# Kernel tuning notes

Measured on AMD Instinct MI355X. Metric: run time of the kernel, lower is better.

## Reference

```python
import jax, jax.numpy as jnp
import numpy as np
import math

B, T, C, H = 4, 2048, 1024, 16
D = C // H  # head dim = 64
W_STD = 0.02


def setup_inputs() -> dict:
    key = jax.random.key(0)
    kx, kw, kb = jax.random.split(key, 3)
    x = jax.random.normal(kx, (B, T, C), dtype=jnp.float32)
    # Linear params stored as [in, 3*in] for x @ W; scaled like typical init
    w_qkv = jax.random.normal(kw, (C, 3 * C), dtype=jnp.float32) * W_STD
    b_qkv = jax.random.normal(kb, (3 * C,), dtype=jnp.float32) * W_STD
    return {"x": x, "w_qkv": w_qkv, "b_qkv": b_qkv}


def reference(x, w_qkv, b_qkv):
    # Fused QKV projection; torch splits as keys, queries, values (in that order)
    qkv = x @ w_qkv + b_qkv                      # [B, T, 3C]
    k, q, v = jnp.split(qkv, 3, axis=-1)          # each [B, T, C]

    def heads(t):  # [B, T, C] -> [B, H, T, D]
        return t.reshape(B, T, H, D).transpose(0, 2, 1, 3)

    k, q, v = heads(k), heads(q), heads(v)
    scale = 1.0 / math.sqrt(D)
    logits = jnp.einsum("bhqd,bhkd->bhqk", q, k) * scale  # [B, H, T, T]
    causal = jnp.tril(jnp.ones((T, T), dtype=bool))
    logits = jnp.where(causal, logits, -jnp.inf)
    probs = jax.nn.softmax(logits, axis=-1)
    y = jnp.einsum("bhqk,bhkd->bhqd", probs, v)   # [B, H, T, D]
    return y.transpose(0, 2, 1, 3).reshape(B, T, C)
```

## Files before the change

### kernel.cpp

```cpp
#include <hip/hip_runtime.h>
#include <hip/hip_bf16.h>

typedef unsigned short ushort_t;
typedef __attribute__((ext_vector_type(4))) short bf16x4_t;
typedef __attribute__((ext_vector_type(8))) short short8;
typedef __attribute__((ext_vector_type(4))) unsigned short ushort4_t;
typedef __attribute__((ext_vector_type(4))) float f32x4;
typedef __attribute__((ext_vector_type(2))) unsigned int uint2_t;
typedef __attribute__((ext_vector_type(4))) unsigned int uint4_t;

#define LOG2E 1.44269504088896340736f

__device__ __forceinline__ unsigned short f2bf(float f) {
    unsigned int u = __float_as_uint(f);
    u += 0x7fffu + ((u >> 16) & 1u);
    return (unsigned short)(u >> 16);
}

__device__ __forceinline__ unsigned int pk2bf(float a, float b) {
    union { __hip_bfloat162 h2; unsigned int u; } cvt;
    cvt.h2 = __float22bfloat162_rn(make_float2(a, b));
    return cvt.u;
}

__device__ __forceinline__ void gl_lds16(const ushort_t* g, ushort_t* l) {
    __builtin_amdgcn_global_load_lds(
        (const __attribute__((address_space(1))) unsigned int*)g,
        (__attribute__((address_space(3))) unsigned int*)l, 16, 0, 0);
}

__device__ __forceinline__ f32x4 mfma16(uint2_t a, uint2_t b, f32x4 c) {
    union { uint2_t u; bf16x4_t s; } ua, ub;
    ua.u = a; ub.u = b;
    return __builtin_amdgcn_mfma_f32_16x16x16bf16_1k(ua.s, ub.s, c, 0, 0, 0);
}

__global__ __launch_bounds__(256) void cvt_x(
    const float* __restrict__ x, ushort_t* __restrict__ xb)
{
    const size_t i = ((size_t)blockIdx.x * 256 + threadIdx.x) * 8;
    const float4 a = *(const float4*)(x + i);
    const float4 b = *(const float4*)(x + i + 4);
    uint4_t o;
    o[0] = pk2bf(a.x, a.y); o[1] = pk2bf(a.z, a.w);
    o[2] = pk2bf(b.x, b.y); o[3] = pk2bf(b.z, b.w);
    *(uint4_t*)(xb + i) = o;
}

__global__ __launch_bounds__(256) void cvt_w(
    const float* __restrict__ w, ushort_t* __restrict__ wt)
{
    __shared__ ushort_t Ts[64][40];
    const int k0 = blockIdx.x * 32, n0 = blockIdx.y * 64;
    const int tid = threadIdx.x;
    const int kr = tid >> 3, nc = (tid & 7) * 8;
    const float* g = w + (size_t)(k0 + kr) * 3072 + n0 + nc;
    const float4 a = *(const float4*)g;
    const float4 b = *(const float4*)(g + 4);
    const float vals[8] = {a.x, a.y, a.z, a.w, b.x, b.y, b.z, b.w};
#pragma unroll
    for (int j = 0; j < 8; ++j) Ts[nc + j][kr] = f2bf(vals[j]);
    __syncthreads();
    const int nr = tid >> 2, kc = (tid & 3) * 8;
    const short8 v = *(const short8*)&Ts[nr][kc];
    *(short8*)(wt + (size_t)(n0 + nr) * 1024 + k0 + kc) = v;
}

__global__ __launch_bounds__(256) void qkv_gemm(
    const ushort_t* __restrict__ xb, const ushort_t* __restrict__ wt,
    const float* __restrict__ bq,
    ushort_t* __restrict__ kws, ushort_t* __restrict__ qws,
    ushort_t* __restrict__ vws)
{
    __shared__ ushort_t As[128 * 32];
    __shared__ ushort_t Bs[128 * 32];

    const int tid  = threadIdx.x;
    const int m0   = blockIdx.x * 128;
    const int n0   = blockIdx.y * 128;
    const int wv   = tid >> 6;
    const int lane = tid & 63;
    const int qr   = lane & 15;
    const int quad = lane >> 4;
    const int wm   = (wv >> 1) * 64;
    const int wn   = (wv & 1) * 64;

    const int lr   = lane >> 2;
    const int scol = (lane & 3) * 8;
    const ushort_t* gA = xb + (size_t)(m0 + wv*32 + lr) * 1024 + scol;
    const ushort_t* gB = wt + (size_t)(n0 + wv*32 + lr) * 1024 + scol;
    ushort_t* lA = As + wv * 32 * 32;
    ushort_t* lB = Bs + wv * 32 * 32;

    f32x4 acc[4][4];
#pragma unroll
    for (int i = 0; i < 4; ++i)
#pragma unroll
        for (int j = 0; j < 4; ++j) acc[i][j] = (f32x4){0.f, 0.f, 0.f, 0.f};

    for (int k0 = 0; k0 < 1024; k0 += 32) {
        __syncthreads();
        gl_lds16(gA + k0,             lA);
        gl_lds16(gA + k0 + 16 * 1024, lA + 16 * 32);
        gl_lds16(gB + k0,             lB);
        gl_lds16(gB + k0 + 16 * 1024, lB + 16 * 32);
        __syncthreads();

        short8 af[4], bfr[4];
#pragma unroll
        for (int i = 0; i < 4; ++i)
            af[i] = *(const short8*)&As[(wm + i*16 + qr) * 32 + quad * 8];
#pragma unroll
        for (int j = 0; j < 4; ++j)
            bfr[j] = *(const short8*)&Bs[(wn + j*16 + qr) * 32 + quad * 8];
#pragma unroll
        for (int i = 0; i < 4; ++i)
#pragma unroll
            for (int j = 0; j < 4; ++j)
                acc[i][j] = __builtin_amdgcn_mfma_f32_16x16x32_bf16(
                    af[i], bfr[j], acc[i][j], 0, 0, 0);
    }

    const int nbase = n0 + wn;
    const int sec   = nbase >> 10;
    const int h     = (nbase & 1023) >> 6;

    if (sec == 2) {
#pragma unroll
        for (int j = 0; j < 4; ++j) {
            const float bias = bq[nbase + j*16 + qr];
            const int d = j*16 + qr;
#pragma unroll
            for (int i = 0; i < 4; ++i) {
                const int m  = m0 + wm + i*16 + quad*4;
                const int bb = m >> 11;
                const int tt = m & 2047;
                ushort4_t pk;
#pragma unroll
                for (int r = 0; r < 4; ++r) pk[r] = f2bf(acc[i][j][r] + bias);
                *(ushort4_t*)&vws[((size_t)(bb*16 + h)*64 + d)*2048 + tt] = pk;
            }
        }
    } else {
        ushort_t* __restrict__ dst = (sec == 0) ? kws : qws;
#pragma unroll
        for (int j = 0; j < 4; ++j) {
            const float bias = bq[nbase + j*16 + qr];
            const int d = j*16 + qr;
#pragma unroll
            for (int i = 0; i < 4; ++i) {
#pragma unroll
                for (int r = 0; r < 4; ++r) {
                    const int m  = m0 + wm + i*16 + quad*4 + r;
                    const int bb = m >> 11;
                    const int tt = m & 2047;
                    dst[(((size_t)(bb*16 + h)) * 2048 + tt) * 64 + d] =
                        f2bf(acc[i][j][r] + bias);
                }
            }
        }
    }
}

__global__ __launch_bounds__(256) void attn_fwd(
    const ushort_t* __restrict__ kws, const ushort_t* __restrict__ qws,
    const ushort_t* __restrict__ vws, float* __restrict__ out)
{
    constexpr int LDK = 72;
    __shared__ ushort_t Ks[2][64 * LDK];
    __shared__ ushort_t Vs[2][64 * LDK];

    const int tid  = threadIdx.x;
    const int wv   = tid >> 6;
    const int lane = tid & 63;
    const int qr   = lane & 15;
    const int quad = lane >> 4;
    const int srow = tid >> 2;
    const int scol = (tid & 3) * 16;
    constexpr float SCL = 0.125f * LOG2E;
    constexpr float CB  = 8.0f;

    const int bh = (int)blockIdx.x >> 3;
    const int jp = (int)blockIdx.x & 7;
    const size_t bhT = (size_t)bh * 2048;
    const ushort_t* kbase = kws + bhT * 64;
    const ushort_t* vbase = vws + (size_t)bh * 64 * 2048;
    const int b = bh >> 4, h = bh & 15;

#pragma unroll 1
    for (int part = 0; part < 2; ++part) {
        const int qt = part ? (15 - jp) : jp;
        const int q0 = qt * 128;

        const int base = q0 + wv*32;
        const int qv0 = base + qr;
        const int qv1 = qv0 + 16;

        const ushort_t* qg0 = qws + (bhT + qv0) * 64;
        const ushort_t* qg1 = qws + (bhT + qv1) * 64;
        const short8 Qb00 = *(const short8*)(qg0 + quad*8);
        const short8 Qb01 = *(const short8*)(qg0 + 32 + quad*8);
        const short8 Qb10 = *(const short8*)(qg1 + quad*8);
        const short8 Qb11 = *(const short8*)(qg1 + 32 + quad*8);

        float l_s[2] = {0.f, 0.f};
        f32x4 Oacc[2][4];
#pragma unroll
        for (int qs = 0; qs < 2; ++qs)
#pragma unroll
            for (int dt = 0; dt < 4; ++dt) Oacc[qs][dt] = (f32x4){0.f,0.f,0.f,0.f};

        const int nkt = 2*qt + 2;
        const int row_max = base + 31;

        short8 kv0, kv1, vv0, vv1;
        {
            const ushort_t* kg = kbase + (size_t)srow * 64 + scol;
            const ushort_t* vg = vbase + (size_t)srow * 2048 + scol;
            kv0 = *(const short8*)(kg);     kv1 = *(const short8*)(kg + 8);
            vv0 = *(const short8*)(vg);     vv1 = *(const short8*)(vg + 8);
        }
        *(short8*)&Ks[0][srow * LDK + scol]     = kv0;
        *(short8*)&Ks[0][srow * LDK + scol + 8] = kv1;
        *(short8*)&Vs[0][srow * LDK + scol]     = vv0;
        *(short8*)&Vs[0][srow * LDK + scol + 8] = vv1;
        __syncthreads();

        for (int kt = 0; kt < nkt; ++kt) {
            const int k0 = kt * 64;
            const int cur = kt & 1;
            const bool more = (kt + 1 < nkt);
            if (more) {
                const ushort_t* kg = kbase + (size_t)(k0 + 64 + srow) * 64 + scol;
                const ushort_t* vg = vbase + (size_t)srow * 2048 + k0 + 64 + scol;
                kv0 = *(const short8*)(kg);   kv1 = *(const short8*)(kg + 8);
                vv0 = *(const short8*)(vg);   vv1 = *(const short8*)(vg + 8);
            }

            if (k0 <= row_max) {
                const ushort_t* Kc = Ks[cur];
                const ushort_t* Vc = Vs[cur];
                const bool diag = (k0 + 63 > base);

                uint2_t pks[2][4];
                float ps0 = 0.f, ps1 = 0.f;
#pragma unroll
                for (int t4 = 0; t4 < 4; ++t4) {
                    const short8 kf0 = *(const short8*)&Kc[(t4*16 + qr)*LDK + quad*8];
                    const short8 kf1 = *(const short8*)&Kc[(t4*16 + qr)*LDK + 32 + quad*8];
                    f32x4 a = (f32x4){0.f,0.f,0.f,0.f};
                    f32x4 bfr = (f32x4){0.f,0.f,0.f,0.f};
                    a   = __builtin_amdgcn_mfma_f32_16x16x32_bf16(kf0, Qb00, a, 0,0,0);
                    a   = __builtin_amdgcn_mfma_f32_16x16x32_bf16(kf1, Qb01, a, 0,0,0);
                    bfr = __builtin_amdgcn_mfma_f32_16x16x32_bf16(kf0, Qb10, bfr, 0,0,0);
                    bfr = __builtin_amdgcn_mfma_f32_16x16x32_bf16(kf1, Qb11, bfr, 0,0,0);
                    if (diag) {
#pragma unroll
                        for (int r = 0; r < 4; ++r) {
                            const int key = k0 + t4*16 + quad*4 + r;
                            if (key > qv0) a[r]   = -INFINITY;
                            if (key > qv1) bfr[r] = -INFINITY;
                        }
                    }
                    float p0[4], p1[4];
#pragma unroll
                    for (int r = 0; r < 4; ++r) {
                        p0[r] = exp2f(__builtin_fmaf(a[r],   SCL, -CB));
                        p1[r] = exp2f(__builtin_fmaf(bfr[r], SCL, -CB));
                        ps0 += p0[r];
                        ps1 += p1[r];
                    }
                    pks[0][t4][0] = pk2bf(p0[0], p0[1]);
                    pks[0][t4][1] = pk2bf(p0[2], p0[3]);
                    pks[1][t4][0] = pk2bf(p1[0], p1[1]);
                    pks[1][t4][1] = pk2bf(p1[2], p1[3]);
                }
                l_s[0] += ps0;
                l_s[1] += ps1;

#pragma unroll
                for (int dt = 0; dt < 4; ++dt) {
#pragma unroll
                    for (int t4 = 0; t4 < 4; ++t4) {
                        const uint2_t vf = *(const uint2_t*)
                            &Vc[(dt*16 + qr)*LDK + t4*16 + quad*4];
                        Oacc[0][dt] = mfma16(pks[0][t4], vf, Oacc[0][dt]);
                        Oacc[1][dt] = mfma16(pks[1][t4], vf, Oacc[1][dt]);
                    }
                }
            }

            if (more) {
                ushort_t* Kn = Ks[cur ^ 1];
                ushort_t* Vn = Vs[cur ^ 1];
                *(short8*)&Kn[srow * LDK + scol]     = kv0;
                *(short8*)&Kn[srow * LDK + scol + 8] = kv1;
                *(short8*)&Vn[srow * LDK + scol]     = vv0;
                *(short8*)&Vn[srow * LDK + scol + 8] = vv1;
            }
            __syncthreads();
        }

#pragma unroll
        for (int qs = 0; qs < 2; ++qs) {
            float lf = l_s[qs];
            lf += __shfl_xor(lf, 16);
            lf += __shfl_xor(lf, 32);
#pragma unroll
            for (int r = 0; r < 4; ++r) {
                const float lr  = __shfl(lf, quad*4 + r);
                const float inv = 1.f / lr;
                const int q = q0 + wv*32 + qs*16 + quad*4 + r;
                float* o = out + ((size_t)(b*2048 + q)) * 1024 + h*64;
#pragma unroll
                for (int dt = 0; dt < 4; ++dt) o[dt*16 + qr] = Oacc[qs][dt][r] * inv;
            }
        }
    }
}

extern "C" void kernel_launch(void* const* d_in, const int* in_sizes, int n_in,
                              void* d_out, int out_size, void* d_ws, size_t ws_size,
                              hipStream_t stream) {
    (void)in_sizes; (void)n_in; (void)out_size; (void)ws_size;
    const float* x  = (const float*)d_in[0];
    const float* w  = (const float*)d_in[1];
    const float* bq = (const float*)d_in[2];
    float* out = (float*)d_out;

    ushort_t* kws = (ushort_t*)d_ws;
    ushort_t* qws = kws + (size_t)8388608;
    ushort_t* vws = qws + (size_t)8388608;
    ushort_t* xb  = vws + (size_t)8388608;
    ushort_t* wt  = xb  + (size_t)8388608;

    cvt_x<<<4096, 256, 0, stream>>>(x, xb);
    cvt_w<<<dim3(32, 48), 256, 0, stream>>>(w, wt);
    qkv_gemm<<<dim3(64, 24), 256, 0, stream>>>(xb, wt, bq, kws, qws, vws);
    attn_fwd<<<512, 256, 0, stream>>>(kws, qws, vws, out);
}
```

Before: 248.3 us.

## Double-buffer QKV GEMM LDS loads and split attention across eight waves

The QKV GEMM now double-buffers its LDS tiles, issuing the global-to-LDS copy for the next K slice before computing the current one, which leaves one barrier per iteration instead of two. The attention kernel moves from 256 to 512 threads, so each wave owns 16 query rows instead of 32 and K/V staging loads are spread over more threads. The P·V MFMA section is wrapped in s_setprio so the scheduler favours matrix work. The costs are twice the GEMM LDS footprint and, in attention, K/V tile reuse per wave is halved while barrier participants double.

```diff
diff --git a/kernel.cpp b/kernel.cpp
--- a/kernel.cpp
+++ b/kernel.cpp
@@ -72,8 +72,8 @@
     ushort_t* __restrict__ kws, ushort_t* __restrict__ qws,
     ushort_t* __restrict__ vws)
 {
-    __shared__ ushort_t As[128 * 32];
-    __shared__ ushort_t Bs[128 * 32];
+    __shared__ ushort_t As[2][128 * 32];
+    __shared__ ushort_t Bs[2][128 * 32];
 
     const int tid  = threadIdx.x;
     const int m0   = blockIdx.x * 128;
@@ -89,8 +89,6 @@
     const int scol = (lane & 3) * 8;
     const ushort_t* gA = xb + (size_t)(m0 + wv*32 + lr) * 1024 + scol;
     const ushort_t* gB = wt + (size_t)(n0 + wv*32 + lr) * 1024 + scol;
-    ushort_t* lA = As + wv * 32 * 32;
-    ushort_t* lB = Bs + wv * 32 * 32;
 
     f32x4 acc[4][4];
 #pragma unroll
@@ -98,27 +96,37 @@
 #pragma unroll
         for (int j = 0; j < 4; ++j) acc[i][j] = (f32x4){0.f, 0.f, 0.f, 0.f};
 
-    for (int k0 = 0; k0 < 1024; k0 += 32) {
-        __syncthreads();
-        gl_lds16(gA + k0,             lA);
-        gl_lds16(gA + k0 + 16 * 1024, lA + 16 * 32);
-        gl_lds16(gB + k0,             lB);
-        gl_lds16(gB + k0 + 16 * 1024, lB + 16 * 32);
-        __syncthreads();
+    gl_lds16(gA,            As[0] + wv*1024);
+    gl_lds16(gA + 16*1024,  As[0] + wv*1024 + 512);
+    gl_lds16(gB,            Bs[0] + wv*1024);
+    gl_lds16(gB + 16*1024,  Bs[0] + wv*1024 + 512);
+    __syncthreads();
+
+    for (int kt = 0; kt < 32; ++kt) {
+        const int cur = kt & 1;
+        if (kt < 31) {
+            const int k1 = (kt + 1) * 32;
+            gl_lds16(gA + k1,           As[cur^1] + wv*1024);
+            gl_lds16(gA + k1 + 16*1024, As[cur^1] + wv*1024 + 512);
+            gl_lds16(gB + k1,           Bs[cur^1] + wv*1024);
+            gl_lds16(gB + k1 + 16*1024, Bs[cur^1] + wv*1024 + 512);
+        }
 
         short8 af[4], bfr[4];
 #pragma unroll
         for (int i = 0; i < 4; ++i)
-            af[i] = *(const short8*)&As[(wm + i*16 + qr) * 32 + quad * 8];
+            af[i] = *(const short8*)&As[cur][(wm + i*16 + qr) * 32 + quad * 8];
 #pragma unroll
         for (int j = 0; j < 4; ++j)
-            bfr[j] = *(const short8*)&Bs[(wn + j*16 + qr) * 32 + quad * 8];
+            bfr[j] = *(const short8*)&Bs[cur][(wn + j*16 + qr) * 32 + quad * 8];
 #pragma unroll
         for (int i = 0; i < 4; ++i)
 #pragma unroll
             for (int j = 0; j < 4; ++j)
                 acc[i][j] = __builtin_amdgcn_mfma_f32_16x16x32_bf16(
                     af[i], bfr[j], acc[i][j], 0, 0, 0);
+
+        __syncthreads();
     }
 
     const int nbase = n0 + wn;
@@ -162,7 +170,7 @@
     }
 }
 
-__global__ __launch_bounds__(256) void attn_fwd(
+__global__ __launch_bounds__(512) void attn_fwd(
     const ushort_t* __restrict__ kws, const ushort_t* __restrict__ qws,
     const ushort_t* __restrict__ vws, float* __restrict__ out)
 {
@@ -175,8 +183,8 @@
     const int lane = tid & 63;
     const int qr   = lane & 15;
     const int quad = lane >> 4;
-    const int srow = tid >> 2;
-    const int scol = (tid & 3) * 16;
+    const int srow = tid >> 3;
+    const int scol = (tid & 7) * 8;
     constexpr float SCL = 0.125f * LOG2E;
     constexpr float CB  = 8.0f;
 
@@ -192,38 +200,30 @@
         const int qt = part ? (15 - jp) : jp;
         const int q0 = qt * 128;
 
-        const int base = q0 + wv*32;
+        const int base = q0 + wv*16;
         const int qv0 = base + qr;
-        const int qv1 = qv0 + 16;
 
         const ushort_t* qg0 = qws + (bhT + qv0) * 64;
-        const ushort_t* qg1 = qws + (bhT + qv1) * 64;
         const short8 Qb00 = *(const short8*)(qg0 + quad*8);
         const short8 Qb01 = *(const short8*)(qg0 + 32 + quad*8);
-        const short8 Qb10 = *(const short8*)(qg1 + quad*8);
-        const short8 Qb11 = *(const short8*)(qg1 + 32 + quad*8);
-
-        float l_s[2] = {0.f, 0.f};
-        f32x4 Oacc[2][4];
-#pragma unroll
-        for (int qs = 0; qs < 2; ++qs)
-#pragma unroll
-            for (int dt = 0; dt < 4; ++dt) Oacc[qs][dt] = (f32x4){0.f,0.f,0.f,0.f};
+
+        float l_s = 0.f;
+        f32x4 Oacc[4];
+#pragma unroll
+        for (int dt = 0; dt < 4; ++dt) Oacc[dt] = (f32x4){0.f,0.f,0.f,0.f};
 
         const int nkt = 2*qt + 2;
-        const int row_max = base + 31;
-
-        short8 kv0, kv1, vv0, vv1;
+        const int row_max = base + 15;
+
+        short8 kv0, vv0;
         {
             const ushort_t* kg = kbase + (size_t)srow * 64 + scol;
             const ushort_t* vg = vbase + (size_t)srow * 2048 + scol;
-            kv0 = *(const short8*)(kg);     kv1 = *(const short8*)(kg + 8);
-            vv0 = *(const short8*)(vg);     vv1 = *(const short8*)(vg + 8);
-        }
-        *(short8*)&Ks[0][srow * LDK + scol]     = kv0;
-        *(short8*)&Ks[0][srow * LDK + scol + 8] = kv1;
-        *(short8*)&Vs[0][srow * LDK + scol]     = vv0;
-        *(short8*)&Vs[0][srow * LDK + scol + 8] = vv1;
+            kv0 = *(const short8*)(kg);
+            vv0 = *(const short8*)(vg);
+        }
+        *(short8*)&Ks[0][srow * LDK + scol] = kv0;
+        *(short8*)&Vs[0][srow * LDK + scol] = vv0;
         __syncthreads();
 
         for (int kt = 0; kt < nkt; ++kt) {
@@ -233,8 +233,8 @@
             if (more) {
                 const ushort_t* kg = kbase + (size_t)(k0 + 64 + srow) * 64 + scol;
                 const ushort_t* vg = vbase + (size_t)srow * 2048 + k0 + 64 + scol;
-                kv0 = *(const short8*)(kg);   kv1 = *(const short8*)(kg + 8);
-                vv0 = *(const short8*)(vg);   vv1 = *(const short8*)(vg + 8);
+                kv0 = *(const short8*)(kg);
+                vv0 = *(const short8*)(vg);
             }
 
             if (k0 <= row_max) {
@@ -242,79 +242,64 @@
                 const ushort_t* Vc = Vs[cur];
                 const bool diag = (k0 + 63 > base);
 
-                uint2_t pks[2][4];
-                float ps0 = 0.f, ps1 = 0.f;
+                uint2_t pks[4];
+                float ps0 = 0.f;
 #pragma unroll
                 for (int t4 = 0; t4 < 4; ++t4) {
                     const short8 kf0 = *(const short8*)&Kc[(t4*16 + qr)*LDK + quad*8];
                     const short8 kf1 = *(const short8*)&Kc[(t4*16 + qr)*LDK + 32 + quad*8];
                     f32x4 a = (f32x4){0.f,0.f,0.f,0.f};
-                    f32x4 bfr = (f32x4){0.f,0.f,0.f,0.f};
-                    a   = __builtin_amdgcn_mfma_f32_16x16x32_bf16(kf0, Qb00, a, 0,0,0);
-                    a   = __builtin_amdgcn_mfma_f32_16x16x32_bf16(kf1, Qb01, a, 0,0,0);
-                    bfr = __builtin_amdgcn_mfma_f32_16x16x32_bf16(kf0, Qb10, bfr, 0,0,0);
-                    bfr = __builtin_amdgcn_mfma_f32_16x16x32_bf16(kf1, Qb11, bfr, 0,0,0);
+                    a = __builtin_amdgcn_mfma_f32_16x16x32_bf16(kf0, Qb00, a, 0,0,0);
+                    a = __builtin_amdgcn_mfma_f32_16x16x32_bf16(kf1, Qb01, a, 0,0,0);
                     if (diag) {
 #pragma unroll
                         for (int r = 0; r < 4; ++r) {
                             const int key = k0 + t4*16 + quad*4 + r;
-                            if (key > qv0) a[r]   = -INFINITY;
-                            if (key > qv1) bfr[r] = -INFINITY;
+                            if (key > qv0) a[r] = -INFINITY;
                         }
                     }
-                    float p0[4], p1[4];
+                    float p0[4];
 #pragma unroll
                     for (int r = 0; r < 4; ++r) {
-                        p0[r] = exp2f(__builtin_fmaf(a[r],   SCL, -CB));
-                        p1[r] = exp2f(__builtin_fmaf(bfr[r], SCL, -CB));
+                        p0[r] = exp2f(__builtin_fmaf(a[r], SCL, -CB));
                         ps0 += p0[r];
-                        ps1 += p1[r];
                     }
-                    pks[0][t4][0] = pk2bf(p0[0], p0[1]);
-                    pks[0][t4][1] = pk2bf(p0[2], p0[3]);
-                    pks[1][t4][0] = pk2bf(p1[0], p1[1]);
-                    pks[1][t4][1] = pk2bf(p1[2], p1[3]);
+                    pks[t4][0] = pk2bf(p0[0], p0[1]);
+                    pks[t4][1] = pk2bf(p0[2], p0[3]);
                 }
-                l_s[0] += ps0;
-                l_s[1] += ps1;
-
+                l_s += ps0;
+
+                __builtin_amdgcn_s_setprio(1);
 #pragma unroll
                 for (int dt = 0; dt < 4; ++dt) {
 #pragma unroll
                     for (int t4 = 0; t4 < 4; ++t4) {
                         const uint2_t vf = *(const uint2_t*)
                             &Vc[(dt*16 + qr)*LDK + t4*16 + quad*4];
-                        Oacc[0][dt] = mfma16(pks[0][t4], vf, Oacc[0][dt]);
-                        Oacc[1][dt] = mfma16(pks[1][t4], vf, Oacc[1][dt]);
+                        Oacc[dt] = mfma16(pks[t4], vf, Oacc[dt]);
                     }
                 }
+                __builtin_amdgcn_s_setprio(0);
             }
 
             if (more) {
-                ushort_t* Kn = Ks[cur ^ 1];
-                ushort_t* Vn = Vs[cur ^ 1];
-                *(short8*)&Kn[srow * LDK + scol]     = kv0;
-                *(short8*)&Kn[srow * LDK + scol + 8] = kv1;
-                *(short8*)&Vn[srow * LDK + scol]     = vv0;
-                *(short8*)&Vn[srow * LDK + scol + 8] = vv1;
+                *(short8*)&Ks[cur ^ 1][srow * LDK + scol] = kv0;
+                *(short8*)&Vs[cur ^ 1][srow * LDK + scol] = vv0;
             }
             __syncthreads();
         }
 
-#pragma unroll
-        for (int qs = 0; qs < 2; ++qs) {
-            float lf = l_s[qs];
-            lf += __shfl_xor(lf, 16);
-            lf += __shfl_xor(lf, 32);
-#pragma unroll
-            for (int r = 0; r < 4; ++r) {
-                const float lr  = __shfl(lf, quad*4 + r);
-                const float inv = 1.f / lr;
-                const int q = q0 + wv*32 + qs*16 + quad*4 + r;
-                float* o = out + ((size_t)(b*2048 + q)) * 1024 + h*64;
-#pragma unroll
-                for (int dt = 0; dt < 4; ++dt) o[dt*16 + qr] = Oacc[qs][dt][r] * inv;
-            }
+        float lf = l_s;
+        lf += __shfl_xor(lf, 16);
+        lf += __shfl_xor(lf, 32);
+#pragma unroll
+        for (int r = 0; r < 4; ++r) {
+            const float lr  = __shfl(lf, quad*4 + r);
+            const float inv = 1.f / lr;
+            const int q = q0 + wv*16 + quad*4 + r;
+            float* o = out + ((size_t)(b*2048 + q)) * 1024 + h*64;
+#pragma unroll
+            for (int dt = 0; dt < 4; ++dt) o[dt*16 + qr] = Oacc[dt][r] * inv;
         }
     }
 }
@@ -337,5 +322,5 @@
     cvt_x<<<4096, 256, 0, stream>>>(x, xb);
     cvt_w<<<dim3(32, 48), 256, 0, stream>>>(w, wt);
     qkv_gemm<<<dim3(64, 24), 256, 0, stream>>>(xb, wt, bq, kws, qws, vws);
-    attn_fwd<<<512, 256, 0, stream>>>(kws, qws, vws, out);
-}
+    attn_fwd<<<512, 512, 0, stream>>>(kws, qws, vws, out);
+}
```

Result: no change. 243.7 us (-1.8%).
